# Kernel tuning notes

Hardware: AMD Instinct MI355X
Metric: run time of the kernel (lower is better)

## Reference

```python
import jax, jax.numpy as jnp
from jax import lax
import numpy as np

B, C, H, W = 32, 64, 128, 128
O, K, KS = 64, 4, 3
HIDDEN = int(C * 0.25) + 1  # 17, per ScaleAwareAttention2d


def setup_inputs() -> dict:
    key = jax.random.key(0)
    ks = jax.random.split(key, 6)
    return {
        "x": jax.random.normal(ks[0], (B, C, H, W), dtype=jnp.float32),
        "scale": jax.random.uniform(ks[1], (1,), dtype=jnp.float32),
        "fc1_w": jax.random.normal(ks[2], (HIDDEN, C), dtype=jnp.float32) * 0.1,
        "fc2_w": jax.random.normal(ks[3], (K, HIDDEN + 2), dtype=jnp.float32) * 0.1,
        "fc2_b": jnp.zeros((K,), dtype=jnp.float32),
        "weight": jax.random.normal(ks[4], (K, O, C, KS, KS), dtype=jnp.float32) * 0.05,
        "bias": jax.random.normal(ks[5], (K, O), dtype=jnp.float32) * 0.05,
    }


def reference(x, scale, fc1_w, fc2_w, fc2_b, weight, bias):
    b = x.shape[0]
    # --- ScaleAwareAttention2d (eval mode -> temperature = 1) ---
    pooled = x.mean(axis=(2, 3))                      # [B, C]  (adaptive avg pool to 1x1)
    h = jax.nn.relu(pooled @ fc1_w.T)                 # [B, HIDDEN]  (1x1 conv, no bias)
    h = jnp.concatenate([h, jnp.ones((b, 2), x.dtype) * scale], axis=1)  # [B, HIDDEN+2]
    logits = h @ fc2_w.T + fc2_b                      # [B, K]
    attn = jax.nn.softmax(logits, axis=1)             # temperature = 1 at inference

    # --- per-sample weight/bias aggregation ---
    agg_w = jnp.einsum('bk,koihw->boihw', attn, weight)  # [B, O, C, KS, KS]
    agg_b = attn @ bias                                   # [B, O]

    # --- per-sample conv (equivalent of F.conv2d with groups = batch) ---
    def one_sample(xi, wi):
        return lax.conv_general_dilated(
            xi[None], wi, window_strides=(1, 1), padding=((1, 1), (1, 1)),
            dimension_numbers=('NCHW', 'OIHW', 'NCHW'))[0]

    out = jax.vmap(one_sample)(x, agg_w)              # [B, O, H, W]
    return out + agg_b[:, :, None, None]
```

## Files before the change

### kernel.cpp

```cpp
#include <hip/hip_runtime.h>
#include <hip/hip_bf16.h>

#define BB 32
#define CC 64
#define HH 128
#define WW 128
#define OO 64
#define KK 4
#define HIDDEN 17
#define HW (HH*WW)

typedef __attribute__((ext_vector_type(8)))  short bf16x8;
typedef __attribute__((ext_vector_type(16))) float f32x16;

typedef __attribute__((address_space(3))) void       lds_void_t;
typedef const __attribute__((address_space(1))) void gbl_void_t;

__device__ __forceinline__ unsigned short f2bf(float f) {
    unsigned u = __float_as_uint(f);
    unsigned r = (u + 0x7FFFu + ((u >> 16) & 1u)) >> 16;
    return (unsigned short)r;
}

__global__ __launch_bounds__(256) void zero_pool_kernel(float* __restrict__ pooled) {
    int i = blockIdx.x * 256 + threadIdx.x;
    if (i < BB * CC) pooled[i] = 0.f;
}

__global__ __launch_bounds__(256) void pool_kernel(const float* __restrict__ x,
                                                   float* __restrict__ pooled) {
    int bc = blockIdx.x;
    const float* p = x + (size_t)bc * HW;
    float s = 0.f;
    for (int i = threadIdx.x; i < HW; i += 256) s += p[i];
    #pragma unroll
    for (int off = 32; off > 0; off >>= 1) s += __shfl_down(s, off, 64);
    __shared__ float warp_s[4];
    int lane = threadIdx.x & 63, wv = threadIdx.x >> 6;
    if (lane == 0) warp_s[wv] = s;
    __syncthreads();
    if (threadIdx.x == 0) {
        float t = warp_s[0] + warp_s[1] + warp_s[2] + warp_s[3];
        pooled[bc] = t * (1.f / (float)HW);
    }
}

__global__ __launch_bounds__(256) void attn_kernel(const float* __restrict__ pooled,
                                                   const float* __restrict__ fc1_w,
                                                   const float* __restrict__ fc2_w,
                                                   const float* __restrict__ fc2_b,
                                                   const float* __restrict__ scale,
                                                   const float* __restrict__ bias,
                                                   float* __restrict__ attn,
                                                   float* __restrict__ agg_b) {
    __shared__ float s_attn[BB * KK];
    int tid = threadIdx.x;
    if (tid < BB) {
        int b = tid;
        const float* pb = pooled + b * CC;
        float h[HIDDEN];
        #pragma unroll
        for (int i = 0; i < HIDDEN; ++i) {
            float s = 0.f;
            for (int c = 0; c < CC; ++c) s += pb[c] * fc1_w[i * CC + c];
            h[i] = fmaxf(s, 0.f);
        }
        float sc = scale[0];
        float logits[KK];
        #pragma unroll
        for (int k = 0; k < KK; ++k) {
            float s = fc2_b[k];
            for (int j = 0; j < HIDDEN; ++j) s += h[j] * fc2_w[k * (HIDDEN + 2) + j];
            s += sc * fc2_w[k * (HIDDEN + 2) + HIDDEN];
            s += sc * fc2_w[k * (HIDDEN + 2) + HIDDEN + 1];
            logits[k] = s;
        }
        float m = fmaxf(fmaxf(logits[0], logits[1]), fmaxf(logits[2], logits[3]));
        float e[KK], tot = 0.f;
        #pragma unroll
        for (int k = 0; k < KK; ++k) { e[k] = __expf(logits[k] - m); tot += e[k]; }
        float inv = 1.f / tot;
        #pragma unroll
        for (int k = 0; k < KK; ++k) {
            float a = e[k] * inv;
            s_attn[b * KK + k] = a;
            attn[b * KK + k] = a;
        }
    }
    __syncthreads();
    for (int i = tid; i < BB * OO; i += blockDim.x) {
        int b = i >> 6;
        int o = i & 63;
        float s = 0.f;
        #pragma unroll
        for (int k = 0; k < KK; ++k) s += s_attn[b * KK + k] * bias[k * OO + o];
        agg_b[i] = s;
    }
}

__global__ __launch_bounds__(256) void aggw_bf_kernel(const float* __restrict__ attn,
                                                      const float* __restrict__ weight,
                                                      unsigned int* __restrict__ wbf) {
    int idx = blockIdx.x * 256 + threadIdx.x;
    const int total = BB * 9 * 2 * 4 * 64 * 4;
    if (idx >= total) return;
    int j2    = idx & 3;
    int lane  = (idx >> 2) & 63;
    int kc    = (idx >> 8) & 3;
    int otile = (idx >> 10) & 1;
    int rest  = idx >> 11;
    int j9    = rest % 9;
    int b     = rest / 9;
    int m   = lane & 31;
    int kh2 = lane >> 5;
    int o   = otile * 32 + m;
    int c0  = kc * 16 + kh2 * 8 + j2 * 2;
    float a0 = attn[b * KK + 0], a1 = attn[b * KK + 1],
          a2 = attn[b * KK + 2], a3 = attn[b * KK + 3];
    float s0 = 0.f, s1 = 0.f;
    s0 += a0 * weight[((0 * OO + o) * CC + c0) * 9 + j9];
    s1 += a0 * weight[((0 * OO + o) * CC + c0 + 1) * 9 + j9];
    s0 += a1 * weight[((1 * OO + o) * CC + c0) * 9 + j9];
    s1 += a1 * weight[((1 * OO + o) * CC + c0 + 1) * 9 + j9];
    s0 += a2 * weight[((2 * OO + o) * CC + c0) * 9 + j9];
    s1 += a2 * weight[((2 * OO + o) * CC + c0 + 1) * 9 + j9];
    s0 += a3 * weight[((3 * OO + o) * CC + c0) * 9 + j9];
    s1 += a3 * weight[((3 * OO + o) * CC + c0 + 1) * 9 + j9];
    wbf[idx] = (unsigned int)f2bf(s0) | ((unsigned int)f2bf(s1) << 16);
}

__global__ __launch_bounds__(256) void xpose_pool_kernel(const float* __restrict__ x,
                                                         unsigned int* __restrict__ xbf32,
                                                         float* __restrict__ pooled) {
    __shared__ float t[64][65];
    __shared__ float s_red[4][64];
    const int y  = blockIdx.x;
    const int b  = blockIdx.y;
    const int x0 = blockIdx.z * 64;
    const int tid = threadIdx.x;
    {
        const int xl = tid & 63;
        const int cs = tid >> 6;
        #pragma unroll
        for (int cc = 0; cc < 16; ++cc) {
            int c = cc * 4 + cs;
            t[c][xl] = x[((size_t)(b * CC + c) * HH + y) * WW + x0 + xl];
        }
    }
    __syncthreads();
    {
        const int c = tid & 63, q = tid >> 6;
        float s = 0.f;
        #pragma unroll
        for (int i = 0; i < 16; ++i) s += t[c][q * 16 + i];
        s_red[q][c] = s;
    }
    {
        const int cp = tid & 31;
        const int xs = tid >> 5;
        const int c0 = cp * 2;
        #pragma unroll
        for (int xx = 0; xx < 8; ++xx) {
            int xl = xx * 8 + xs;
            int xg = x0 + xl;
            unsigned int pack = (unsigned int)f2bf(t[c0][xl]) |
                                ((unsigned int)f2bf(t[c0 + 1][xl]) << 16);
            int cps = cp ^ (((xg + 1) & 7) << 2);
            xbf32[(((size_t)b * HH + y) * WW + xg) * 32 + cps] = pack;
        }
    }
    __syncthreads();
    if (tid < CC) {
        float s = s_red[0][tid] + s_red[1][tid] + s_red[2][tid] + s_red[3][tid];
        atomicAdd(pooled + b * CC + tid, s * (1.f / (float)HW));
    }
}

#define LROW 16640
__global__ __launch_bounds__(256, 3) void conv_mfma_kernel(const short* __restrict__ xbf,
                                                           const short* __restrict__ wbf,
                                                           const float* __restrict__ agg_b,
                                                           float* __restrict__ out) {
    __shared__ __attribute__((aligned(16))) char ldsbuf[3 * LROW];
    unsigned int* lds32 = (unsigned int*)ldsbuf;

    const int s    = blockIdx.x;
    const int y    = ((s & 7) << 4) | (s >> 3);
    const int b    = blockIdx.y;
    const int tid  = threadIdx.x;
    const int lane = tid & 63;
    const int w    = tid >> 6;

    if (tid < 192) {
        int r = tid / 64;
        int q = tid - r * 64;
        int word = (q < 32) ? (r * (LROW/4) + q)
                            : (r * (LROW/4) + 129 * 32 + (q - 32));
        lds32[word] = 0u;
    }
    {
        const short* growb = xbf + (size_t)b * HH * WW * CC;
        #pragma unroll
        for (int i = 0; i < 12; ++i) {
            int call = w * 12 + i;
            int r   = call >> 4;
            int seg = call & 15;
            int iy  = y - 1 + r;
            if (iy >= 0 && iy < HH) {
                const short* g = growb + (size_t)iy * (WW * CC) + seg * 512 + lane * 8;
                char* lp = ldsbuf + r * LROW + 128 + seg * 1024;
                __builtin_amdgcn_global_load_lds((gbl_void_t*)g, (lds_void_t*)lp, 16, 0, 0);
            }
        }
    }
    if (y == 0)   for (int i = tid; i < 4096; i += 256) lds32[32 + i] = 0u;
    if (y == 127) for (int i = tid; i < 4096; i += 256) lds32[2 * (LROW/4) + 32 + i] = 0u;
    __syncthreads();

    const int otile = w & 1;
    const int o0    = otile * 32;
    const int x0    = (w >> 1) * 64;
    const int m     = lane & 31;
    const int kh2   = lane >> 5;
    const int cbase = kh2 * 16;

    f32x16 acc0 = {0,0,0,0,0,0,0,0,0,0,0,0,0,0,0,0};
    f32x16 acc1 = {0,0,0,0,0,0,0,0,0,0,0,0,0,0,0,0};

    const char* ldsc = ldsbuf;
    #pragma unroll
    for (int j9 = 0; j9 < 9; ++j9) {
        const int kh = j9 / 3, kw = j9 % 3;
        const short* Aj = wbf + (((size_t)b * 9 + j9) * 2 + otile) * 2048 + lane * 8;
        const int p0  = x0 + m + kw;
        const int sw  = ((m + kw) & 7) << 4;
        const int a0b = kh * LROW + p0 * 128;
        const int a1b = a0b + 32 * 128;
        #pragma unroll
        for (int kc = 0; kc < 4; ++kc) {
            bf16x8 a  = *(const bf16x8*)(Aj + kc * 512);
            const int c_off = (cbase + kc * 32) ^ sw;
            bf16x8 b0 = *(const bf16x8*)(ldsc + a0b + c_off);
            bf16x8 b1 = *(const bf16x8*)(ldsc + a1b + c_off);
            acc0 = __builtin_amdgcn_mfma_f32_32x32x16_bf16(a, b0, acc0, 0, 0, 0);
            acc1 = __builtin_amdgcn_mfma_f32_32x32x16_bf16(a, b1, acc1, 0, 0, 0);
        }
    }

    #pragma unroll
    for (int r = 0; r < 16; ++r) {
        int o = o0 + (r & 3) + 8 * (r >> 2) + 4 * kh2;
        float bias = agg_b[b * OO + o];
        size_t base = ((size_t)(b * OO + o) * HH + y) * WW;
        out[base + x0 + m]      = acc0[r] + bias;
        out[base + x0 + 32 + m] = acc1[r] + bias;
    }
}

__global__ __launch_bounds__(256) void aggw_kernel(const float* __restrict__ attn,
                                                   const float* __restrict__ weight,
                                                   float* __restrict__ agg_w) {
    int idx = blockIdx.x * 256 + threadIdx.x;
    const int total = BB * CC * OO * 9;
    if (idx >= total) return;
    int j  = idx % 9;
    int t  = idx / 9;
    int o  = t & 63;
    int t2 = t >> 6;
    int c  = t2 & 63;
    int b  = t2 >> 6;
    float s = 0.f;
    #pragma unroll
    for (int k = 0; k < KK; ++k)
        s += attn[b * KK + k] * weight[((k * OO + o) * CC + c) * 9 + j];
    agg_w[idx] = s;
}

__global__ __launch_bounds__(256) void conv_kernel(const float* __restrict__ x,
                                                   const float* __restrict__ agg_w,
                                                   const float* __restrict__ agg_b,
                                                   float* __restrict__ out) {
    __shared__ float s_in[2][18 * 20];
    const int tid = threadIdx.x;
    const int tx = tid & 15, ty = tid >> 4;
    const int b  = blockIdx.z;
    const int o0 = blockIdx.y * 8;
    const int sy = (blockIdx.x >> 3) * 16;
    const int sx = (blockIdx.x & 7) * 16;

    const float* __restrict__ xb = x + (size_t)b * CC * HW;
    const float* __restrict__ wb = agg_w + (size_t)b * CC * OO * 9;

    float acc[8];
    #pragma unroll
    for (int o = 0; o < 8; ++o) acc[o] = agg_b[b * OO + o0 + o];

    auto load_ch = [&](int c, float* dst) {
        for (int i = tid; i < 18 * 18; i += 256) {
            int r   = i / 18;
            int col = i - r * 18;
            int gy = sy + r - 1;
            int gx = sx + col - 1;
            float v = 0.f;
            if (gy >= 0 && gy < HH && gx >= 0 && gx < WW)
                v = xb[c * HW + gy * WW + gx];
            dst[r * 20 + col] = v;
        }
    };

    load_ch(0, s_in[0]);
    __syncthreads();

    for (int c = 0; c < CC; ++c) {
        const int buf = c & 1;
        if (c + 1 < CC) load_ch(c + 1, s_in[buf ^ 1]);
        float in[3][3];
        #pragma unroll
        for (int kh = 0; kh < 3; ++kh)
            #pragma unroll
            for (int kw = 0; kw < 3; ++kw)
                in[kh][kw] = s_in[buf][(ty + kh) * 20 + (tx + kw)];
        const float* __restrict__ wc = wb + (c * OO + o0) * 9;
        #pragma unroll
        for (int o = 0; o < 8; ++o)
            #pragma unroll
            for (int kh = 0; kh < 3; ++kh)
                #pragma unroll
                for (int kw = 0; kw < 3; ++kw)
                    acc[o] += in[kh][kw] * wc[o * 9 + kh * 3 + kw];
        __syncthreads();
    }

    const int oy = sy + ty, ox = sx + tx;
    #pragma unroll
    for (int o = 0; o < 8; ++o)
        out[((size_t)(b * OO + o0 + o) * HH + oy) * WW + ox] = acc[o];
}

extern "C" void kernel_launch(void* const* d_in, const int* in_sizes, int n_in,
                              void* d_out, int out_size, void* d_ws, size_t ws_size,
                              hipStream_t stream) {
    const float* x      = (const float*)d_in[0];
    const float* scale  = (const float*)d_in[1];
    const float* fc1_w  = (const float*)d_in[2];
    const float* fc2_w  = (const float*)d_in[3];
    const float* fc2_b  = (const float*)d_in[4];
    const float* weight = (const float*)d_in[5];
    const float* bias   = (const float*)d_in[6];
    float* out = (float*)d_out;

    const size_t XBF_BYTES = (size_t)BB * HH * WW * CC * 2;
    const size_t WBF_BYTES = (size_t)BB * 9 * OO * CC * 2;
    const size_t NEED = XBF_BYTES + WBF_BYTES + (2048 + 128 + 2048) * 4 + 256;

    if (ws_size >= NEED) {
        short*        xbf   = (short*)d_ws;
        unsigned int* xbf32 = (unsigned int*)d_ws;
        unsigned int* wbf32 = (unsigned int*)((char*)d_ws + XBF_BYTES);
        short*        wbf   = (short*)wbf32;
        float*        fls   = (float*)((char*)d_ws + XBF_BYTES + WBF_BYTES);
        float* pooled = fls;
        float* attn   = fls + 2048;
        float* agg_b  = fls + 2048 + 128;

        zero_pool_kernel<<<8, 256, 0, stream>>>(pooled);
        xpose_pool_kernel<<<dim3(HH, BB, 2), 256, 0, stream>>>(x, xbf32, pooled);
        attn_kernel<<<1, 256, 0, stream>>>(pooled, fc1_w, fc2_w, fc2_b, scale, bias, attn, agg_b);
        const int aggw_total = BB * 9 * 2 * 4 * 64 * 4;
        aggw_bf_kernel<<<(aggw_total + 255) / 256, 256, 0, stream>>>(attn, weight, wbf32);
        conv_mfma_kernel<<<dim3(HH, BB), 256, 0, stream>>>(xbf, wbf, agg_b, out);
    } else {
        float* ws     = (float*)d_ws;
        float* attn   = ws;
        float* agg_b  = ws + 128;
        float* pooled = ws + 128 + 2048;
        float* agg_w  = ws + 128 + 2048 + 2048;
        pool_kernel<<<BB * CC, 256, 0, stream>>>(x, pooled);
        attn_kernel<<<1, 256, 0, stream>>>(pooled, fc1_w, fc2_w, fc2_b, scale, bias, attn, agg_b);
        const int aggw_total = BB * CC * OO * 9;
        aggw_kernel<<<(aggw_total + 255) / 256, 256, 0, stream>>>(attn, weight, agg_w);
        conv_kernel<<<dim3(64, 8, BB), 256, 0, stream>>>(x, agg_w, agg_b, out);
    }
}
```

Measured before the change: 338.3 us.

## Fuse attention into weight aggregation and vectorize transpose-pool loads/stores

Merges the single-block attention kernel into the weight-aggregation kernel. Each block recomputes the attention for 4 samples and stages a tile of the expert weights in shared memory, so weight reads are coalesced float4 loads reused across the samples. This removes one launch and the strided scalar weight gathers. The transpose/pool kernel now reads x with float4 loads into a channel-minor LDS tile and writes 16-byte packed bf16 groups with the same XOR swizzle. The cost is redundant fc1/fc2 math per block and only 64 blocks for the aggregation.

```diff
diff --git a/kernel.cpp b/kernel.cpp
--- a/kernel.cpp
+++ b/kernel.cpp
@@ -98,53 +98,125 @@
     }
 }
 
-__global__ __launch_bounds__(256) void aggw_bf_kernel(const float* __restrict__ attn,
-                                                      const float* __restrict__ weight,
-                                                      unsigned int* __restrict__ wbf) {
-    int idx = blockIdx.x * 256 + threadIdx.x;
-    const int total = BB * 9 * 2 * 4 * 64 * 4;
-    if (idx >= total) return;
-    int j2    = idx & 3;
-    int lane  = (idx >> 2) & 63;
-    int kc    = (idx >> 8) & 3;
-    int otile = (idx >> 10) & 1;
-    int rest  = idx >> 11;
-    int j9    = rest % 9;
-    int b     = rest / 9;
-    int m   = lane & 31;
-    int kh2 = lane >> 5;
-    int o   = otile * 32 + m;
-    int c0  = kc * 16 + kh2 * 8 + j2 * 2;
-    float a0 = attn[b * KK + 0], a1 = attn[b * KK + 1],
-          a2 = attn[b * KK + 2], a3 = attn[b * KK + 3];
-    float s0 = 0.f, s1 = 0.f;
-    s0 += a0 * weight[((0 * OO + o) * CC + c0) * 9 + j9];
-    s1 += a0 * weight[((0 * OO + o) * CC + c0 + 1) * 9 + j9];
-    s0 += a1 * weight[((1 * OO + o) * CC + c0) * 9 + j9];
-    s1 += a1 * weight[((1 * OO + o) * CC + c0 + 1) * 9 + j9];
-    s0 += a2 * weight[((2 * OO + o) * CC + c0) * 9 + j9];
-    s1 += a2 * weight[((2 * OO + o) * CC + c0 + 1) * 9 + j9];
-    s0 += a3 * weight[((3 * OO + o) * CC + c0) * 9 + j9];
-    s1 += a3 * weight[((3 * OO + o) * CC + c0 + 1) * 9 + j9];
-    wbf[idx] = (unsigned int)f2bf(s0) | ((unsigned int)f2bf(s1) << 16);
+__global__ __launch_bounds__(256) void aggw_fused_kernel(const float* __restrict__ pooled,
+                                                         const float* __restrict__ fc1_w,
+                                                         const float* __restrict__ fc2_w,
+                                                         const float* __restrict__ fc2_b,
+                                                         const float* __restrict__ scale,
+                                                         const float* __restrict__ bias,
+                                                         const float* __restrict__ weight,
+                                                         float* __restrict__ agg_b,
+                                                         unsigned int* __restrict__ wbf) {
+    __shared__ float4 sw4[128 * 37];
+    __shared__ float  sh[4][20];
+    __shared__ float  sa[4][4];
+    const float* swf = (const float*)sw4;
+
+    const int tid = threadIdx.x;
+    const int b4  = blockIdx.x;
+    const int oty = blockIdx.y;
+    const int kcz = blockIdx.z;
+
+    {
+        const float4* w4 = (const float4*)weight;
+        #pragma unroll
+        for (int it = 0; it < 18; ++it) {
+            int i   = tid + it * 256;
+            int seg = i / 36;
+            int off = i - seg * 36;
+            int k   = seg >> 5;
+            int o   = seg & 31;
+            sw4[seg * 37 + off] = w4[(size_t)(k * 64 + oty * 32 + o) * 144 + kcz * 36 + off];
+        }
+    }
+    const int wv = tid >> 6, lane = tid & 63;
+    const int bb = b4 * 4 + wv;
+    if (lane < HIDDEN) {
+        const float* pb = pooled + bb * CC;
+        const float* f1 = fc1_w + lane * CC;
+        float s = 0.f;
+        #pragma unroll
+        for (int c = 0; c < CC; ++c) s += pb[c] * f1[c];
+        sh[wv][lane] = fmaxf(s, 0.f);
+    }
+    __syncthreads();
+    if (lane == 0) {
+        float sc = scale[0];
+        float lg[KK];
+        #pragma unroll
+        for (int k = 0; k < KK; ++k) {
+            float s = fc2_b[k];
+            #pragma unroll
+            for (int j = 0; j < HIDDEN; ++j) s += sh[wv][j] * fc2_w[k * (HIDDEN + 2) + j];
+            s += sc * fc2_w[k * (HIDDEN + 2) + HIDDEN];
+            s += sc * fc2_w[k * (HIDDEN + 2) + HIDDEN + 1];
+            lg[k] = s;
+        }
+        float m = fmaxf(fmaxf(lg[0], lg[1]), fmaxf(lg[2], lg[3]));
+        float e[KK], tot = 0.f;
+        #pragma unroll
+        for (int k = 0; k < KK; ++k) { e[k] = __expf(lg[k] - m); tot += e[k]; }
+        float inv = 1.f / tot;
+        #pragma unroll
+        for (int k = 0; k < KK; ++k) sa[wv][k] = e[k] * inv;
+    }
+    __syncthreads();
+
+    if (oty == 0 && kcz == 0) {
+        int bl = tid >> 6, o = tid & 63;
+        float s = 0.f;
+        #pragma unroll
+        for (int k = 0; k < KK; ++k) s += sa[bl][k] * bias[k * OO + o];
+        agg_b[(b4 * 4 + bl) * OO + o] = s;
+    }
+
+    const int lane6 = tid >> 2;
+    const int j2    = tid & 3;
+    const int m     = lane6 & 31;
+    const int kh2   = lane6 >> 5;
+    const int cl    = kh2 * 8 + j2 * 2;
+    #pragma unroll
+    for (int bl = 0; bl < 4; ++bl) {
+        const int b = b4 * 4 + bl;
+        const float a0 = sa[bl][0], a1 = sa[bl][1], a2 = sa[bl][2], a3 = sa[bl][3];
+        #pragma unroll
+        for (int j9 = 0; j9 < 9; ++j9) {
+            float s0, s1;
+            {
+                const float* p0 = swf + (0 * 32 + m) * 148 + cl * 9 + j9;
+                const float* p1 = swf + (1 * 32 + m) * 148 + cl * 9 + j9;
+                const float* p2 = swf + (2 * 32 + m) * 148 + cl * 9 + j9;
+                const float* p3 = swf + (3 * 32 + m) * 148 + cl * 9 + j9;
+                s0 = a0 * p0[0] + a1 * p1[0] + a2 * p2[0] + a3 * p3[0];
+                s1 = a0 * p0[9] + a1 * p1[9] + a2 * p2[9] + a3 * p3[9];
+            }
+            wbf[(((size_t)b * 9 + j9) * 8 + oty * 4 + kcz) * 256 + tid] =
+                (unsigned int)f2bf(s0) | ((unsigned int)f2bf(s1) << 16);
+        }
+    }
 }
 
 __global__ __launch_bounds__(256) void xpose_pool_kernel(const float* __restrict__ x,
                                                          unsigned int* __restrict__ xbf32,
                                                          float* __restrict__ pooled) {
-    __shared__ float t[64][65];
+    __shared__ float t2[64][68];
     __shared__ float s_red[4][64];
     const int y  = blockIdx.x;
     const int b  = blockIdx.y;
     const int x0 = blockIdx.z * 64;
     const int tid = threadIdx.x;
     {
-        const int xl = tid & 63;
-        const int cs = tid >> 6;
-        #pragma unroll
-        for (int cc = 0; cc < 16; ++cc) {
-            int c = cc * 4 + cs;
-            t[c][xl] = x[((size_t)(b * CC + c) * HH + y) * WW + x0 + xl];
+        const int xq = tid & 15;
+        const int cb = (tid >> 4) * 4;
+        #pragma unroll
+        for (int i = 0; i < 4; ++i) {
+            const int c = cb + i;
+            const float4 v = *(const float4*)(x + (size_t)(b * CC + c) * HW
+                                                + (size_t)y * WW + x0 + xq * 4);
+            t2[xq * 4 + 0][c] = v.x;
+            t2[xq * 4 + 1][c] = v.y;
+            t2[xq * 4 + 2][c] = v.z;
+            t2[xq * 4 + 3][c] = v.w;
         }
     }
     __syncthreads();
@@ -152,21 +224,24 @@
         const int c = tid & 63, q = tid >> 6;
         float s = 0.f;
         #pragma unroll
-        for (int i = 0; i < 16; ++i) s += t[c][q * 16 + i];
+        for (int i = 0; i < 16; ++i) s += t2[q * 16 + i][c];
         s_red[q][c] = s;
     }
     {
-        const int cp = tid & 31;
-        const int xs = tid >> 5;
-        const int c0 = cp * 2;
-        #pragma unroll
-        for (int xx = 0; xx < 8; ++xx) {
-            int xl = xx * 8 + xs;
-            int xg = x0 + xl;
-            unsigned int pack = (unsigned int)f2bf(t[c0][xl]) |
-                                ((unsigned int)f2bf(t[c0 + 1][xl]) << 16);
-            int cps = cp ^ (((xg + 1) & 7) << 2);
-            xbf32[(((size_t)b * HH + y) * WW + xg) * 32 + cps] = pack;
+        const int xl  = tid >> 2;
+        const int xg  = x0 + xl;
+        const int key = (xg + 1) & 7;
+        unsigned int* dst = xbf32 + ((size_t)(b * HH + y) * WW + xg) * 32;
+        #pragma unroll
+        for (int gg = 0; gg < 2; ++gg) {
+            const int g = (tid & 3) + gg * 4;
+            const float* src = &t2[xl][g * 8];
+            uint4 pk;
+            pk.x = (unsigned int)f2bf(src[0]) | ((unsigned int)f2bf(src[1]) << 16);
+            pk.y = (unsigned int)f2bf(src[2]) | ((unsigned int)f2bf(src[3]) << 16);
+            pk.z = (unsigned int)f2bf(src[4]) | ((unsigned int)f2bf(src[5]) << 16);
+            pk.w = (unsigned int)f2bf(src[6]) | ((unsigned int)f2bf(src[7]) << 16);
+            *(uint4*)(dst + (g ^ key) * 4) = pk;
         }
     }
     __syncthreads();
@@ -360,14 +435,12 @@
         short*        wbf   = (short*)wbf32;
         float*        fls   = (float*)((char*)d_ws + XBF_BYTES + WBF_BYTES);
         float* pooled = fls;
-        float* attn   = fls + 2048;
         float* agg_b  = fls + 2048 + 128;
 
         zero_pool_kernel<<<8, 256, 0, stream>>>(pooled);
         xpose_pool_kernel<<<dim3(HH, BB, 2), 256, 0, stream>>>(x, xbf32, pooled);
-        attn_kernel<<<1, 256, 0, stream>>>(pooled, fc1_w, fc2_w, fc2_b, scale, bias, attn, agg_b);
-        const int aggw_total = BB * 9 * 2 * 4 * 64 * 4;
-        aggw_bf_kernel<<<(aggw_total + 255) / 256, 256, 0, stream>>>(attn, weight, wbf32);
+        aggw_fused_kernel<<<dim3(8, 2, 4), 256, 0, stream>>>(pooled, fc1_w, fc2_w, fc2_b,
+                                                             scale, bias, weight, agg_b, wbf32);
         conv_mfma_kernel<<<dim3(HH, BB), 256, 0, stream>>>(xbf, wbf, agg_b, out);
     } else {
         float* ws     = (float*)d_ws;
```

Result: faster. 301.4 us (-10.9%).
